# Performance work log

Hardware: AMD Instinct MI355X
Metric: run time of the kernel (lower is better)

Reference implementation:

```python
import jax, jax.numpy as jnp
import numpy as np

SG_SLOPE = 20.0  # fast_sigmoid surrogate slope
THRESHOLD = 1.0

@jax.custom_vjp
def spike_fn(v):
    # Heaviside spike with fast-sigmoid surrogate gradient
    return (v > 0).astype(v.dtype)

def _spike_fwd(v):
    return spike_fn(v), v

def _spike_bwd(v, g):
    return (g / (SG_SLOPE * jnp.abs(v) + 1.0) ** 2,)

spike_fn.defvjp(_spike_fwd, _spike_bwd)

def setup_inputs() -> dict:
    key = jax.random.key(0)
    T, IN, H, HEADS, O = 8192, 192, 1024, 5, 2
    dt = 0.004
    sp = float(np.log1p(np.exp(0.5413)))  # softplus(param) ~= 1.0
    tau_syn_h, tau_mem_h = 0.01 * sp, 0.02 * sp
    tau_syn_r = np.array([0.01, 0.02, 0.05, 0.1, 0.2]) * sp
    tau_mem_r = np.array([0.02, 0.05, 0.1, 0.2, 0.5]) * sp
    k1, k2, k3, k4 = jax.random.split(key, 4)
    x = jax.random.normal(k1, (T, IN), jnp.float32)
    W_in = jax.random.normal(k2, (H, IN), jnp.float32) / np.sqrt(IN)
    V = jax.random.normal(k3, (H, H), jnp.float32) / np.sqrt(H)
    b_rec = jnp.zeros((H,), jnp.float32)
    W_out = jax.random.normal(k4, (HEADS, O, H), jnp.float32) / np.sqrt(H)
    return {
        "x": x, "W_in": W_in, "V": V, "b_rec": b_rec, "W_out": W_out,
        "alpha_h": jnp.float32(np.exp(-dt / tau_syn_h)),
        "beta_h": jnp.float32(np.exp(-dt / tau_mem_h)),
        "alpha_r": jnp.asarray(np.exp(-dt / tau_syn_r), jnp.float32),
        "beta_r": jnp.asarray(np.exp(-dt / tau_mem_r), jnp.float32),
    }

def reference(x, W_in, V, b_rec, W_out, alpha_h, beta_h, alpha_r, beta_r):
    H = W_in.shape[0]
    HEADS, O, _ = W_out.shape
    dt_f32 = x.dtype

    def step(carry, x_t):
        inp_prev, spk, syn_h, mem_h, syn_r, mem_r = carry
        # hidden RSynaptic (note: fc_hidden consumes the PREVIOUS input, one-step delay)
        cur = W_in @ inp_prev + V @ spk + b_rec
        syn_h_new = alpha_h * syn_h + cur
        reset = jax.lax.stop_gradient(spk)  # zero-reset uses previous spike, detached
        mem_h_new = (beta_h * mem_h + syn_h_new) * (1.0 - reset)
        spk_new = spike_fn(mem_h_new - THRESHOLD)
        # readout heads consume the PREVIOUS hidden spike (pre-update)
        r_in = jnp.einsum("hoc,c->ho", W_out, spk)  # [HEADS, 2]
        syn_r_new = alpha_r[:, None] * syn_r + r_in
        mem_r_new = beta_r[:, None] * mem_r + syn_r_new  # reset_mechanism='none'
        out = mem_r_new.mean(axis=0)  # average over readout heads
        return (x_t, spk_new, syn_h_new, mem_h_new, syn_r_new, mem_r_new), out

    init = (
        jnp.zeros_like(x[0]),
        jnp.zeros((H,), dt_f32),
        jnp.zeros((H,), dt_f32),
        jnp.zeros((H,), dt_f32),
        jnp.zeros((HEADS, O), dt_f32),
        jnp.zeros((HEADS, O), dt_f32),
    )
    _, preds = jax.lax.scan(step, init, x)
    return preds  # [T, 2]
```

## Files before the change

### kernel.cpp

```cpp
#include <hip/hip_runtime.h>
#include <hip/hip_bf16.h>


constexpr int T_STEPS = 8192;
constexpr int IN_DIM  = 192;
constexpr int H_DIM   = 1024;
constexpr int NBLK    = 32;
constexpr int RING    = 4;

__global__ void k_clear(unsigned int* __restrict__ p, int n) {
    int i = blockIdx.x * blockDim.x + threadIdx.x;
    if (i < n) p[i] = 0u;
}

__global__ __launch_bounds__(576, 1) void k_phase1(
    const float* __restrict__ x,
    const float* __restrict__ W_in,
    const float* __restrict__ V,
    const float* __restrict__ b_rec,
    const float* __restrict__ alpha_h_p,
    const float* __restrict__ beta_h_p,
    unsigned long long* __restrict__ mbox,
    uint2* __restrict__ raster)
{
    const int tid   = threadIdx.x;
    const int blk   = blockIdx.x;
    const int w     = tid >> 6;
    const int l     = tid & 63;
    const bool syncw = (w == 8);
    const int r_local = l >> 4;
    const int cg      = l & 15;
    const int row   = (blk << 5) + (w << 2) + r_local;

    __shared__ unsigned int       bits_lds[2][NBLK];
    __shared__ unsigned long long combine[2];

    if (tid < NBLK) { bits_lds[0][tid] = 0u; bits_lds[1][tid] = 0u; }
    if (tid == 0)   { combine[0] = 0ull; combine[1] = 0ull; }

    float4 vfrag[16];
    float  wfrag[12];
    float  b_r = 0.f;
    if (!syncw) {
        const float4* vp = (const float4*)(V + (size_t)row * H_DIM + cg * 64);
        #pragma unroll
        for (int i = 0; i < 16; ++i) vfrag[i] = vp[i];
        const float* wp = W_in + row * IN_DIM + cg * 12;
        #pragma unroll
        for (int i = 0; i < 12; ++i) wfrag[i] = wp[i];
        b_r = b_rec[row];
    }
    const float ah = alpha_h_p[0];
    const float bh = beta_h_p[0];

    const float* xptr = x + cg * 12;
    float xr[12];
    #pragma unroll
    for (int i = 0; i < 12; ++i) xr[i] = 0.0f;

    float syn = 0.f, mem = 0.f, prev = 0.f;

    __syncthreads();

    for (int t = 0; t < T_STEPS; ++t) {
        const int rs  = (t + 1) & 1;
        const int wsl = t & 1;

        if (!syncw) {
            const float4* xp4 = (const float4*)xptr;
            float4 f0 = xp4[0], f1 = xp4[1], f2 = xp4[2];

            unsigned int b0 = bits_lds[rs][2 * cg];
            unsigned int b1 = bits_lds[rs][2 * cg + 1];

            float a0 = 0.f, a1 = 0.f;
            #pragma unroll
            for (int i = 0; i < 8; ++i) {
                a0 = fmaf((float)((b0 >> (4 * i + 0)) & 1u), vfrag[i].x, a0);
                a0 = fmaf((float)((b0 >> (4 * i + 1)) & 1u), vfrag[i].y, a0);
                a0 = fmaf((float)((b0 >> (4 * i + 2)) & 1u), vfrag[i].z, a0);
                a0 = fmaf((float)((b0 >> (4 * i + 3)) & 1u), vfrag[i].w, a0);
                a1 = fmaf((float)((b1 >> (4 * i + 0)) & 1u), vfrag[8 + i].x, a1);
                a1 = fmaf((float)((b1 >> (4 * i + 1)) & 1u), vfrag[8 + i].y, a1);
                a1 = fmaf((float)((b1 >> (4 * i + 2)) & 1u), vfrag[8 + i].z, a1);
                a1 = fmaf((float)((b1 >> (4 * i + 3)) & 1u), vfrag[8 + i].w, a1);
            }
            #pragma unroll
            for (int i = 0; i < 12; ++i) a0 = fmaf(wfrag[i], xr[i], a0);
            float acc = a0 + a1;

            #pragma unroll
            for (int m = 1; m < 16; m <<= 1) acc += __shfl_xor(acc, m, 64);

            float cur = acc + b_r;
            syn = fmaf(ah, syn, cur);
            mem = fmaf(bh, mem, syn) * (1.0f - prev);
            float spk = (mem > 1.0f) ? 1.0f : 0.0f;
            prev = spk;

            unsigned long long bal = __ballot(spk > 0.5f);
            unsigned int isLast = 0u, bitsAll = 0u;
            if (l == 0) {
                unsigned int nib = (unsigned int)(bal & 1ull)
                                 | ((unsigned int)((bal >> 16) & 1ull) << 1)
                                 | ((unsigned int)((bal >> 32) & 1ull) << 2)
                                 | ((unsigned int)((bal >> 48) & 1ull) << 3);
                unsigned long long add =
                    (1ull << 32) | ((unsigned long long)nib << (4 * w));
                unsigned long long old = __hip_atomic_fetch_add(&combine[wsl], add,
                        __ATOMIC_RELAXED, __HIP_MEMORY_SCOPE_WORKGROUP);
                unsigned long long nv = old + add;
                if ((nv >> 32) == 8ull) { isLast = 1u; bitsAll = (unsigned int)nv; }
            }
            isLast = __shfl(isLast, 0, 64);
            if (isLast) {
                unsigned int bits = __shfl(bitsAll, 0, 64);
                unsigned int want = (unsigned int)(t + 1);
                unsigned int w0 = (want << 16) | (bits & 0xffffu);
                unsigned int w1 = (want << 16) | (bits >> 16);
                unsigned long long pack =
                    (unsigned long long)w0 | ((unsigned long long)w1 << 32);
                if (l < NBLK && l != blk) {
                    __hip_atomic_store(
                        &mbox[(size_t)(((t & (RING - 1)) * NBLK + l) * NBLK + blk)],
                        pack, __ATOMIC_RELAXED, __HIP_MEMORY_SCOPE_AGENT);
                }
                if (l == 0) {
                    raster[(size_t)t * NBLK + blk] = make_uint2(w0, w1);
                    bits_lds[wsl][blk] = bits;
                    combine[wsl] = 0ull;
                }
            }

            #pragma unroll
            for (int i = 0; i < 4; ++i) {
                xr[i]     = (&f0.x)[i];
                xr[4 + i] = (&f1.x)[i];
                xr[8 + i] = (&f2.x)[i];
            }
            xptr += IN_DIM;
        } else {
            if (t + 1 < T_STEPS) {
                const bool act = (l < NBLK) && (l != blk);
                const unsigned int want = (unsigned int)(t + 1);
                const unsigned long long* p =
                    &mbox[(size_t)(((t & (RING - 1)) * NBLK + blk) * NBLK + l)];
                unsigned long long vv = 0ull;
                bool ok = !act;
                if (act) {
                    vv = __hip_atomic_load(p, __ATOMIC_RELAXED,
                                           __HIP_MEMORY_SCOPE_AGENT);
                    ok = (((vv >> 16) & 0xffffull) == want) && ((vv >> 48) == want);
                }
                while (__any(!ok)) {
                    if (!ok) {
                        vv = __hip_atomic_load(p, __ATOMIC_RELAXED,
                                               __HIP_MEMORY_SCOPE_AGENT);
                        ok = (((vv >> 16) & 0xffffull) == want) && ((vv >> 48) == want);
                    }
                }
                if (act)
                    bits_lds[wsl][l] = (unsigned int)(vv & 0xffffull)
                                     | ((unsigned int)((vv >> 32) & 0xffffull) << 16);
            }
        }

        asm volatile("s_waitcnt lgkmcnt(0)" ::: "memory");
        __builtin_amdgcn_s_barrier();
        __builtin_amdgcn_sched_barrier(0);
    }
}

__global__ __launch_bounds__(256, 1) void k_readout_mm(
    const uint2* __restrict__ raster,
    const float* __restrict__ W_out,
    float* __restrict__ R)
{
    __shared__ float wlds[10 * 1033];
    for (int i = threadIdx.x; i < 10 * 1024; i += 256) {
        int r = i >> 10, c = i & 1023;
        wlds[r * 1033 + c] = W_out[i];
    }
    __syncthreads();

    int tid = threadIdx.x;
    if (tid >= 250) return;
    int tl = tid / 10, rowr = tid - tl * 10;
    int t = blockIdx.x * 25 + tl;
    if (t >= T_STEPS) return;

    float acc = 0.f;
    if (t > 0) {
        const uint2* wp = raster + (size_t)(t - 1) * NBLK;
        const float* wr = &wlds[rowr * 1033];
        for (int ww = 0; ww < NBLK; ++ww) {
            uint2 v = wp[ww];
            unsigned int bits = (v.x & 0xffffu) | ((v.y & 0xffffu) << 16);
            const float* wb = wr + ww * 32;
            #pragma unroll
            for (int j = 0; j < 32; ++j)
                acc = fmaf((float)((bits >> j) & 1u), wb[j], acc);
        }
    }
    R[t * 10 + rowr] = acc;
}

__global__ void k_scan(const float* __restrict__ R,
                       const float* __restrict__ alpha_r,
                       const float* __restrict__ beta_r,
                       float* __restrict__ memr_all)
{
    int lane = threadIdx.x;
    bool act = lane < 10;
    float a = act ? alpha_r[lane >> 1] : 0.f;
    float b = act ? beta_r[lane >> 1] : 0.f;
    float syn = 0.f, mem = 0.f;
    constexpr int PF = 8;
    float buf[PF];
    #pragma unroll
    for (int i = 0; i < PF; ++i) buf[i] = act ? R[i * 10 + lane] : 0.f;

    for (int tb = 0; tb < T_STEPS; tb += PF) {
        #pragma unroll
        for (int i = 0; i < PF; ++i) {
            int t = tb + i;
            syn = fmaf(a, syn, buf[i]);
            mem = fmaf(b, mem, syn);
            if (act) memr_all[t * 10 + lane] = mem;
            int tn = t + PF;
            buf[i] = (act && tn < T_STEPS) ? R[tn * 10 + lane] : 0.f;
        }
    }
}

__global__ void k_mean(const float* __restrict__ memr_all, float* __restrict__ out) {
    int g = blockIdx.x * blockDim.x + threadIdx.x;
    if (g >= T_STEPS * 2) return;
    int t = g >> 1, o = g & 1;
    const float* m = memr_all + t * 10 + o;
    out[g] = 0.2f * (m[0] + m[2] + m[4] + m[6] + m[8]);
}

extern "C" void kernel_launch(void* const* d_in, const int* in_sizes, int n_in,
                              void* d_out, int out_size, void* d_ws, size_t ws_size,
                              hipStream_t stream) {
    (void)in_sizes; (void)n_in; (void)out_size; (void)ws_size;
    const float* x       = (const float*)d_in[0];
    const float* W_in    = (const float*)d_in[1];
    const float* V       = (const float*)d_in[2];
    const float* b_rec   = (const float*)d_in[3];
    const float* W_out   = (const float*)d_in[4];
    const float* alpha_h = (const float*)d_in[5];
    const float* beta_h  = (const float*)d_in[6];
    const float* alpha_r = (const float*)d_in[7];
    const float* beta_r  = (const float*)d_in[8];
    float* out = (float*)d_out;

    char* wsb = (char*)d_ws;
    unsigned long long* mbox = (unsigned long long*)wsb;
    uint2* raster  = (uint2*)(wsb + RING * NBLK * NBLK * 8);
    float* Rbuf    = (float*)(wsb + RING * NBLK * NBLK * 8
                              + (size_t)T_STEPS * NBLK * 8);
    float* memr_all = Rbuf + (size_t)T_STEPS * 10;

    int nclr = RING * NBLK * NBLK * 2;
    k_clear<<<(nclr + 255) / 256, 256, 0, stream>>>((unsigned int*)mbox, nclr);
    k_phase1<<<NBLK, 576, 0, stream>>>(x, W_in, V, b_rec, alpha_h, beta_h,
                                       mbox, raster);
    k_readout_mm<<<(T_STEPS + 24) / 25, 256, 0, stream>>>(raster, W_out, Rbuf);
    k_scan<<<1, 64, 0, stream>>>(Rbuf, alpha_r, beta_r, memr_all);
    k_mean<<<(T_STEPS * 2 + 255) / 256, 256, 0, stream>>>(memr_all, out);
}
```

Baseline: 19.12 ms.

## Replace per-step workgroup barrier with LDS ready-flag handshake and deeper ring

Removes the per-timestep s_barrier between the sync wave and the compute waves. Readiness is now signalled through a packed LDS flag: the sync wave publishes how many steps of remote bits have arrived, and the last compute wave publishes its local bits. Spike bits are held in a 4-slot LDS ring so the sync wave can run ahead of the compute waves. Spin loops contain dummy FMAs, apparently to keep the waves busy while waiting, and the relaxed ordering adds some risk of correctness issues under memory reordering.

Result: faster. 17.78 ms (-7.0%).

```diff
diff --git a/kernel.cpp b/kernel.cpp
--- a/kernel.cpp
+++ b/kernel.cpp
@@ -32,11 +32,15 @@
     const int cg      = l & 15;
     const int row   = (blk << 5) + (w << 2) + r_local;
 
-    __shared__ unsigned int       bits_lds[2][NBLK];
+    __shared__ unsigned int       bits_lds[RING][NBLK];
     __shared__ unsigned long long combine[2];
-
-    if (tid < NBLK) { bits_lds[0][tid] = 0u; bits_lds[1][tid] = 0u; }
-    if (tid == 0)   { combine[0] = 0ull; combine[1] = 0ull; }
+    __shared__ unsigned long long rdyPack;
+
+    for (int i = tid; i < RING * NBLK; i += 576)
+        ((unsigned int*)bits_lds)[i] = 0u;
+    if (tid == 0) { combine[0] = 0ull; combine[1] = 0ull; rdyPack = 0ull; }
+
+    unsigned int* rp = (unsigned int*)&rdyPack;
 
     float4 vfrag[16];
     float  wfrag[12];
@@ -53,25 +57,69 @@
     const float ah = alpha_h_p[0];
     const float bh = beta_h_p[0];
 
-    const float* xptr = x + cg * 12;
-    float xr[12];
-    #pragma unroll
-    for (int i = 0; i < 12; ++i) xr[i] = 0.0f;
-
-    float syn = 0.f, mem = 0.f, prev = 0.f;
-
     __syncthreads();
 
-    for (int t = 0; t < T_STEPS; ++t) {
-        const int rs  = (t + 1) & 1;
-        const int wsl = t & 1;
-
-        if (!syncw) {
+    float u0 = 1.02f, u1 = 1.03f, u2 = 1.05f, u3 = 1.07f;
+    const float bc = 1.0000001f, bd = 1e-30f;
+
+    if (syncw) {
+        const bool act = (l < NBLK) && (l != blk);
+        for (int t = 0; t < T_STEPS - 1; ++t) {
+            const unsigned int want = (unsigned int)(t + 1);
+            const unsigned long long good =
+                ((unsigned long long)want << 16) | ((unsigned long long)want << 48);
+            const unsigned long long* p =
+                &mbox[(size_t)(((t & (RING - 1)) * NBLK + blk) * NBLK + l)];
+            unsigned long long vv = act
+                ? __hip_atomic_load(p, __ATOMIC_RELAXED, __HIP_MEMORY_SCOPE_AGENT)
+                : good;
+            bool ok = (((vv >> 16) & 0xffffull) == want) && ((vv >> 48) == want);
+            while (__any(!ok)) {
+                if (!ok)
+                    vv = __hip_atomic_load(p, __ATOMIC_RELAXED,
+                                           __HIP_MEMORY_SCOPE_AGENT);
+                #pragma unroll
+                for (int i = 0; i < 8; ++i) {
+                    u0 = fmaf(u0, bc, bd); u1 = fmaf(u1, bc, bd);
+                    u2 = fmaf(u2, bc, bd); u3 = fmaf(u3, bc, bd);
+                }
+                ok = (((vv >> 16) & 0xffffull) == want) && ((vv >> 48) == want);
+            }
+            if (act)
+                bits_lds[t & (RING - 1)][l] =
+                    (unsigned int)(vv & 0xffffull)
+                    | ((unsigned int)((vv >> 32) & 0xffffull) << 16);
+            if (l == 0)
+                __hip_atomic_store(&rp[0], (unsigned int)(t + 1),
+                                   __ATOMIC_RELEASE, __HIP_MEMORY_SCOPE_WORKGROUP);
+        }
+    } else {
+        const float* xptr = x + cg * 12;
+        float xr[12];
+        #pragma unroll
+        for (int i = 0; i < 12; ++i) xr[i] = 0.0f;
+        float syn = 0.f, mem = 0.f, prev = 0.f;
+
+        for (int t = 0; t < T_STEPS; ++t) {
             const float4* xp4 = (const float4*)xptr;
             float4 f0 = xp4[0], f1 = xp4[1], f2 = xp4[2];
 
-            unsigned int b0 = bits_lds[rs][2 * cg];
-            unsigned int b1 = bits_lds[rs][2 * cg + 1];
+            unsigned long long rv = __hip_atomic_load(&rdyPack, __ATOMIC_ACQUIRE,
+                                        __HIP_MEMORY_SCOPE_WORKGROUP);
+            while ((unsigned int)rv < (unsigned int)t ||
+                   (unsigned int)(rv >> 32) < (unsigned int)t) {
+                #pragma unroll
+                for (int i = 0; i < 4; ++i) {
+                    u0 = fmaf(u0, bc, bd); u1 = fmaf(u1, bc, bd);
+                    u2 = fmaf(u2, bc, bd); u3 = fmaf(u3, bc, bd);
+                }
+                rv = __hip_atomic_load(&rdyPack, __ATOMIC_ACQUIRE,
+                                       __HIP_MEMORY_SCOPE_WORKGROUP);
+            }
+
+            const int slot = (t + RING - 1) & (RING - 1);
+            unsigned int b0 = bits_lds[slot][2 * cg];
+            unsigned int b1 = bits_lds[slot][2 * cg + 1];
 
             float a0 = 0.f, a1 = 0.f;
             #pragma unroll
@@ -107,8 +155,8 @@
                                  | ((unsigned int)((bal >> 48) & 1ull) << 3);
                 unsigned long long add =
                     (1ull << 32) | ((unsigned long long)nib << (4 * w));
-                unsigned long long old = __hip_atomic_fetch_add(&combine[wsl], add,
-                        __ATOMIC_RELAXED, __HIP_MEMORY_SCOPE_WORKGROUP);
+                unsigned long long old = __hip_atomic_fetch_add(&combine[t & 1],
+                        add, __ATOMIC_RELAXED, __HIP_MEMORY_SCOPE_WORKGROUP);
                 unsigned long long nv = old + add;
                 if ((nv >> 32) == 8ull) { isLast = 1u; bitsAll = (unsigned int)nv; }
             }
@@ -116,19 +164,22 @@
             if (isLast) {
                 unsigned int bits = __shfl(bitsAll, 0, 64);
                 unsigned int want = (unsigned int)(t + 1);
-                unsigned int w0 = (want << 16) | (bits & 0xffffu);
-                unsigned int w1 = (want << 16) | (bits >> 16);
+                unsigned int w0t = (want << 16) | (bits & 0xffffu);
+                unsigned int w1t = (want << 16) | (bits >> 16);
                 unsigned long long pack =
-                    (unsigned long long)w0 | ((unsigned long long)w1 << 32);
+                    (unsigned long long)w0t | ((unsigned long long)w1t << 32);
                 if (l < NBLK && l != blk) {
                     __hip_atomic_store(
                         &mbox[(size_t)(((t & (RING - 1)) * NBLK + l) * NBLK + blk)],
                         pack, __ATOMIC_RELAXED, __HIP_MEMORY_SCOPE_AGENT);
                 }
                 if (l == 0) {
-                    raster[(size_t)t * NBLK + blk] = make_uint2(w0, w1);
-                    bits_lds[wsl][blk] = bits;
-                    combine[wsl] = 0ull;
+                    raster[(size_t)t * NBLK + blk] = make_uint2(w0t, w1t);
+                    bits_lds[t & (RING - 1)][blk] = bits;
+                    combine[t & 1] = 0ull;
+                    __hip_atomic_store(&rp[1], (unsigned int)(t + 1),
+                                       __ATOMIC_RELEASE,
+                                       __HIP_MEMORY_SCOPE_WORKGROUP);
                 }
             }
 
@@ -139,36 +190,9 @@
                 xr[8 + i] = (&f2.x)[i];
             }
             xptr += IN_DIM;
-        } else {
-            if (t + 1 < T_STEPS) {
-                const bool act = (l < NBLK) && (l != blk);
-                const unsigned int want = (unsigned int)(t + 1);
-                const unsigned long long* p =
-                    &mbox[(size_t)(((t & (RING - 1)) * NBLK + blk) * NBLK + l)];
-                unsigned long long vv = 0ull;
-                bool ok = !act;
-                if (act) {
-                    vv = __hip_atomic_load(p, __ATOMIC_RELAXED,
-                                           __HIP_MEMORY_SCOPE_AGENT);
-                    ok = (((vv >> 16) & 0xffffull) == want) && ((vv >> 48) == want);
-                }
-                while (__any(!ok)) {
-                    if (!ok) {
-                        vv = __hip_atomic_load(p, __ATOMIC_RELAXED,
-                                               __HIP_MEMORY_SCOPE_AGENT);
-                        ok = (((vv >> 16) & 0xffffull) == want) && ((vv >> 48) == want);
-                    }
-                }
-                if (act)
-                    bits_lds[wsl][l] = (unsigned int)(vv & 0xffffull)
-                                     | ((unsigned int)((vv >> 32) & 0xffffull) << 16);
-            }
-        }
-
-        asm volatile("s_waitcnt lgkmcnt(0)" ::: "memory");
-        __builtin_amdgcn_s_barrier();
-        __builtin_amdgcn_sched_barrier(0);
-    }
+        }
+    }
+    asm volatile("" :: "v"(u0), "v"(u1), "v"(u2), "v"(u3));
 }
 
 __global__ __launch_bounds__(256, 1) void k_readout_mm(
```

## Co-locate recurrent workers on one XCD and poll mailboxes directly from compute waves

Applied to the files above, without the earlier changes.

Launches 256 blocks and picks the first XCD to gather 32 blocks; only those 32 run the recurrence, so all inter-block mailbox traffic stays within one XCD's L2. The dedicated sync wave and per-step workgroup barrier are removed. Every compute wave now polls the mailbox itself with sc0 loads and distributes the spike words by shuffle, and each block also writes its own slot. Spin loops add dummy FMAs, and the selection protocol relies on hardware XCC IDs and on 32 blocks fitting on one XCD.

New measurement: 26.76 ms. +40.0%, slower.

```diff
diff --git a/kernel.cpp b/kernel.cpp
--- a/kernel.cpp
+++ b/kernel.cpp
@@ -5,15 +5,16 @@
 constexpr int T_STEPS = 8192;
 constexpr int IN_DIM  = 192;
 constexpr int H_DIM   = 1024;
-constexpr int NBLK    = 32;
+constexpr int NWORK   = 32;
 constexpr int RING    = 4;
+constexpr int NSEL    = 256;
 
 __global__ void k_clear(unsigned int* __restrict__ p, int n) {
     int i = blockIdx.x * blockDim.x + threadIdx.x;
     if (i < n) p[i] = 0u;
 }
 
-__global__ __launch_bounds__(576, 1) void k_phase1(
+__global__ __launch_bounds__(512, 1) void k_phase1(
     const float* __restrict__ x,
     const float* __restrict__ W_in,
     const float* __restrict__ V,
@@ -21,37 +22,59 @@
     const float* __restrict__ alpha_h_p,
     const float* __restrict__ beta_h_p,
     unsigned long long* __restrict__ mbox,
+    unsigned int* __restrict__ sel,
     uint2* __restrict__ raster)
 {
-    const int tid   = threadIdx.x;
-    const int blk   = blockIdx.x;
-    const int w     = tid >> 6;
-    const int l     = tid & 63;
-    const bool syncw = (w == 8);
+    const int tid = threadIdx.x;
+    __shared__ unsigned int sh_rank, sh_win;
+    __shared__ unsigned long long combine[2];
+
+    unsigned int xcd;
+    asm("s_getreg_b32 %0, hwreg(HW_REG_XCC_ID)" : "=s"(xcd));
+    xcd &= 7u;
+
+    if (tid == 0) {
+        combine[0] = 0ull; combine[1] = 0ull;
+        unsigned int r = __hip_atomic_fetch_add(&sel[xcd], 1u,
+                             __ATOMIC_RELAXED, __HIP_MEMORY_SCOPE_AGENT);
+        sh_rank = r;
+        if (r == NWORK - 1) {
+            unsigned int exp0 = 0u;
+            __hip_atomic_compare_exchange_strong(&sel[8], &exp0, xcd + 1u,
+                __ATOMIC_RELEASE, __ATOMIC_RELAXED, __HIP_MEMORY_SCOPE_AGENT);
+        }
+        unsigned int wv;
+        do {
+            wv = __hip_atomic_load(&sel[8], __ATOMIC_ACQUIRE,
+                                   __HIP_MEMORY_SCOPE_AGENT);
+        } while (wv == 0u);
+        sh_win = wv;
+    }
+    __syncthreads();
+    if (sh_win != xcd + 1u || sh_rank >= (unsigned)NWORK) return;
+    const int me = (int)sh_rank;
+
+    const int w  = tid >> 6;
+    const int l  = tid & 63;
     const int r_local = l >> 4;
     const int cg      = l & 15;
-    const int row   = (blk << 5) + (w << 2) + r_local;
-
-    __shared__ unsigned int       bits_lds[2][NBLK];
-    __shared__ unsigned long long combine[2];
-
-    if (tid < NBLK) { bits_lds[0][tid] = 0u; bits_lds[1][tid] = 0u; }
-    if (tid == 0)   { combine[0] = 0ull; combine[1] = 0ull; }
+    const int row = (me << 5) + (w << 2) + r_local;
 
     float4 vfrag[16];
-    float  wfrag[12];
-    float  b_r = 0.f;
-    if (!syncw) {
+    {
         const float4* vp = (const float4*)(V + (size_t)row * H_DIM + cg * 64);
         #pragma unroll
         for (int i = 0; i < 16; ++i) vfrag[i] = vp[i];
+    }
+    float wfrag[12];
+    {
         const float* wp = W_in + row * IN_DIM + cg * 12;
         #pragma unroll
         for (int i = 0; i < 12; ++i) wfrag[i] = wp[i];
-        b_r = b_rec[row];
-    }
-    const float ah = alpha_h_p[0];
-    const float bh = beta_h_p[0];
+    }
+    const float b_r = b_rec[row];
+    const float ah  = alpha_h_p[0];
+    const float bh  = beta_h_p[0];
 
     const float* xptr = x + cg * 12;
     float xr[12];
@@ -60,115 +83,121 @@
 
     float syn = 0.f, mem = 0.f, prev = 0.f;
 
+    float u0 = 1.02f, u1 = 1.03f;
+    const float bc = 1.0000001f, bd = 1e-30f;
+
     __syncthreads();
 
     for (int t = 0; t < T_STEPS; ++t) {
-        const int rs  = (t + 1) & 1;
+        const float4* xp4 = (const float4*)xptr;
+        float4 f0 = xp4[0], f1 = xp4[1], f2 = xp4[2];
+
+        unsigned long long word = 0ull;
+        if (t > 0) {
+            const unsigned int want = (unsigned int)t;
+            const unsigned long long* pa =
+                &mbox[((size_t)((t - 1) & (RING - 1)) * NWORK + me) * NWORK + (l & 31)];
+            unsigned long long vv;
+            asm volatile("global_load_dwordx2 %0, %1, off sc0\n\t"
+                         "s_waitcnt vmcnt(0)"
+                         : "=&v"(vv) : "v"(pa) : "memory");
+            bool ok = (((unsigned int)(vv >> 16) & 0xffffu) == want) &&
+                      ((unsigned int)(vv >> 48) == want);
+            int spins = 0;
+            while (__any(!ok)) {
+                if (!ok) {
+                    if (++spins <= 6) {
+                        asm volatile("global_load_dwordx2 %0, %1, off sc0\n\t"
+                                     "s_waitcnt vmcnt(0)"
+                                     : "=&v"(vv) : "v"(pa) : "memory");
+                    } else {
+                        vv = __hip_atomic_load(pa, __ATOMIC_RELAXED,
+                                               __HIP_MEMORY_SCOPE_AGENT);
+                    }
+                    ok = (((unsigned int)(vv >> 16) & 0xffffu) == want) &&
+                         ((unsigned int)(vv >> 48) == want);
+                }
+                u0 = fmaf(u0, bc, bd); u1 = fmaf(u1, bc, bd);
+            }
+            word = vv;
+        }
+        unsigned long long p0 = __shfl(word, 2 * cg, 64);
+        unsigned long long p1 = __shfl(word, 2 * cg + 1, 64);
+        unsigned int b0 = ((unsigned int)p0 & 0xffffu)
+                        | (((unsigned int)(p0 >> 32) & 0xffffu) << 16);
+        unsigned int b1 = ((unsigned int)p1 & 0xffffu)
+                        | (((unsigned int)(p1 >> 32) & 0xffffu) << 16);
+
+        float a0 = 0.f, a1 = 0.f;
+        #pragma unroll
+        for (int i = 0; i < 8; ++i) {
+            a0 = fmaf((float)((b0 >> (4 * i + 0)) & 1u), vfrag[i].x, a0);
+            a0 = fmaf((float)((b0 >> (4 * i + 1)) & 1u), vfrag[i].y, a0);
+            a0 = fmaf((float)((b0 >> (4 * i + 2)) & 1u), vfrag[i].z, a0);
+            a0 = fmaf((float)((b0 >> (4 * i + 3)) & 1u), vfrag[i].w, a0);
+            a1 = fmaf((float)((b1 >> (4 * i + 0)) & 1u), vfrag[8 + i].x, a1);
+            a1 = fmaf((float)((b1 >> (4 * i + 1)) & 1u), vfrag[8 + i].y, a1);
+            a1 = fmaf((float)((b1 >> (4 * i + 2)) & 1u), vfrag[8 + i].z, a1);
+            a1 = fmaf((float)((b1 >> (4 * i + 3)) & 1u), vfrag[8 + i].w, a1);
+        }
+        #pragma unroll
+        for (int i = 0; i < 12; ++i) a0 = fmaf(wfrag[i], xr[i], a0);
+        float acc = a0 + a1;
+
+        #pragma unroll
+        for (int m = 1; m < 16; m <<= 1) acc += __shfl_xor(acc, m, 64);
+
+        float cur = acc + b_r;
+        syn = fmaf(ah, syn, cur);
+        mem = fmaf(bh, mem, syn) * (1.0f - prev);
+        float spk = (mem > 1.0f) ? 1.0f : 0.0f;
+        prev = spk;
+
         const int wsl = t & 1;
-
-        if (!syncw) {
-            const float4* xp4 = (const float4*)xptr;
-            float4 f0 = xp4[0], f1 = xp4[1], f2 = xp4[2];
-
-            unsigned int b0 = bits_lds[rs][2 * cg];
-            unsigned int b1 = bits_lds[rs][2 * cg + 1];
-
-            float a0 = 0.f, a1 = 0.f;
-            #pragma unroll
-            for (int i = 0; i < 8; ++i) {
-                a0 = fmaf((float)((b0 >> (4 * i + 0)) & 1u), vfrag[i].x, a0);
-                a0 = fmaf((float)((b0 >> (4 * i + 1)) & 1u), vfrag[i].y, a0);
-                a0 = fmaf((float)((b0 >> (4 * i + 2)) & 1u), vfrag[i].z, a0);
-                a0 = fmaf((float)((b0 >> (4 * i + 3)) & 1u), vfrag[i].w, a0);
-                a1 = fmaf((float)((b1 >> (4 * i + 0)) & 1u), vfrag[8 + i].x, a1);
-                a1 = fmaf((float)((b1 >> (4 * i + 1)) & 1u), vfrag[8 + i].y, a1);
-                a1 = fmaf((float)((b1 >> (4 * i + 2)) & 1u), vfrag[8 + i].z, a1);
-                a1 = fmaf((float)((b1 >> (4 * i + 3)) & 1u), vfrag[8 + i].w, a1);
+        unsigned long long bal = __ballot(spk > 0.5f);
+        unsigned int isLast = 0u, bitsAll = 0u;
+        if (l == 0) {
+            unsigned int nib = (unsigned int)(bal & 1ull)
+                             | ((unsigned int)((bal >> 16) & 1ull) << 1)
+                             | ((unsigned int)((bal >> 32) & 1ull) << 2)
+                             | ((unsigned int)((bal >> 48) & 1ull) << 3);
+            unsigned long long add =
+                (1ull << 32) | ((unsigned long long)nib << (4 * w));
+            unsigned long long old = __hip_atomic_fetch_add(&combine[wsl], add,
+                    __ATOMIC_RELAXED, __HIP_MEMORY_SCOPE_WORKGROUP);
+            unsigned long long nv = old + add;
+            if ((nv >> 32) == 8ull) { isLast = 1u; bitsAll = (unsigned int)nv; }
+        }
+        isLast = __shfl(isLast, 0, 64);
+        if (isLast) {
+            unsigned int bits = __shfl(bitsAll, 0, 64);
+            unsigned int want = (unsigned int)(t + 1);
+            unsigned int w0t = (want << 16) | (bits & 0xffffu);
+            unsigned int w1t = (want << 16) | (bits >> 16);
+            unsigned long long pack =
+                (unsigned long long)w0t | ((unsigned long long)w1t << 32);
+            if (l == 0) combine[wsl] = 0ull;
+            asm volatile("s_waitcnt lgkmcnt(0)" ::: "memory");
+            if (l < NWORK) {
+                unsigned long long* ps =
+                    &mbox[((size_t)(t & (RING - 1)) * NWORK + l) * NWORK + me];
+                asm volatile("global_store_dwordx2 %0, %1, off sc0"
+                             :: "v"(ps), "v"(pack) : "memory");
+                __hip_atomic_store(ps, pack, __ATOMIC_RELAXED,
+                                   __HIP_MEMORY_SCOPE_AGENT);
             }
-            #pragma unroll
-            for (int i = 0; i < 12; ++i) a0 = fmaf(wfrag[i], xr[i], a0);
-            float acc = a0 + a1;
-
-            #pragma unroll
-            for (int m = 1; m < 16; m <<= 1) acc += __shfl_xor(acc, m, 64);
-
-            float cur = acc + b_r;
-            syn = fmaf(ah, syn, cur);
-            mem = fmaf(bh, mem, syn) * (1.0f - prev);
-            float spk = (mem > 1.0f) ? 1.0f : 0.0f;
-            prev = spk;
-
-            unsigned long long bal = __ballot(spk > 0.5f);
-            unsigned int isLast = 0u, bitsAll = 0u;
-            if (l == 0) {
-                unsigned int nib = (unsigned int)(bal & 1ull)
-                                 | ((unsigned int)((bal >> 16) & 1ull) << 1)
-                                 | ((unsigned int)((bal >> 32) & 1ull) << 2)
-                                 | ((unsigned int)((bal >> 48) & 1ull) << 3);
-                unsigned long long add =
-                    (1ull << 32) | ((unsigned long long)nib << (4 * w));
-                unsigned long long old = __hip_atomic_fetch_add(&combine[wsl], add,
-                        __ATOMIC_RELAXED, __HIP_MEMORY_SCOPE_WORKGROUP);
-                unsigned long long nv = old + add;
-                if ((nv >> 32) == 8ull) { isLast = 1u; bitsAll = (unsigned int)nv; }
-            }
-            isLast = __shfl(isLast, 0, 64);
-            if (isLast) {
-                unsigned int bits = __shfl(bitsAll, 0, 64);
-                unsigned int want = (unsigned int)(t + 1);
-                unsigned int w0 = (want << 16) | (bits & 0xffffu);
-                unsigned int w1 = (want << 16) | (bits >> 16);
-                unsigned long long pack =
-                    (unsigned long long)w0 | ((unsigned long long)w1 << 32);
-                if (l < NBLK && l != blk) {
-                    __hip_atomic_store(
-                        &mbox[(size_t)(((t & (RING - 1)) * NBLK + l) * NBLK + blk)],
-                        pack, __ATOMIC_RELAXED, __HIP_MEMORY_SCOPE_AGENT);
-                }
-                if (l == 0) {
-                    raster[(size_t)t * NBLK + blk] = make_uint2(w0, w1);
-                    bits_lds[wsl][blk] = bits;
-                    combine[wsl] = 0ull;
-                }
-            }
-
-            #pragma unroll
-            for (int i = 0; i < 4; ++i) {
-                xr[i]     = (&f0.x)[i];
-                xr[4 + i] = (&f1.x)[i];
-                xr[8 + i] = (&f2.x)[i];
-            }
-            xptr += IN_DIM;
-        } else {
-            if (t + 1 < T_STEPS) {
-                const bool act = (l < NBLK) && (l != blk);
-                const unsigned int want = (unsigned int)(t + 1);
-                const unsigned long long* p =
-                    &mbox[(size_t)(((t & (RING - 1)) * NBLK + blk) * NBLK + l)];
-                unsigned long long vv = 0ull;
-                bool ok = !act;
-                if (act) {
-                    vv = __hip_atomic_load(p, __ATOMIC_RELAXED,
-                                           __HIP_MEMORY_SCOPE_AGENT);
-                    ok = (((vv >> 16) & 0xffffull) == want) && ((vv >> 48) == want);
-                }
-                while (__any(!ok)) {
-                    if (!ok) {
-                        vv = __hip_atomic_load(p, __ATOMIC_RELAXED,
-                                               __HIP_MEMORY_SCOPE_AGENT);
-                        ok = (((vv >> 16) & 0xffffull) == want) && ((vv >> 48) == want);
-                    }
-                }
-                if (act)
-                    bits_lds[wsl][l] = (unsigned int)(vv & 0xffffull)
-                                     | ((unsigned int)((vv >> 32) & 0xffffull) << 16);
-            }
-        }
-
-        asm volatile("s_waitcnt lgkmcnt(0)" ::: "memory");
-        __builtin_amdgcn_s_barrier();
-        __builtin_amdgcn_sched_barrier(0);
-    }
+            if (l == 0) raster[(size_t)t * NWORK + me] = make_uint2(w0t, w1t);
+        }
+
+        #pragma unroll
+        for (int i = 0; i < 4; ++i) {
+            xr[i]     = (&f0.x)[i];
+            xr[4 + i] = (&f1.x)[i];
+            xr[8 + i] = (&f2.x)[i];
+        }
+        xptr += IN_DIM;
+    }
+    asm volatile("" :: "v"(u0), "v"(u1));
 }
 
 __global__ __launch_bounds__(256, 1) void k_readout_mm(
@@ -191,9 +220,9 @@
 
     float acc = 0.f;
     if (t > 0) {
-        const uint2* wp = raster + (size_t)(t - 1) * NBLK;
+        const uint2* wp = raster + (size_t)(t - 1) * NWORK;
         const float* wr = &wlds[rowr * 1033];
-        for (int ww = 0; ww < NBLK; ++ww) {
+        for (int ww = 0; ww < NWORK; ++ww) {
             uint2 v = wp[ww];
             unsigned int bits = (v.x & 0xffffu) | ((v.y & 0xffffu) << 16);
             const float* wb = wr + ww * 32;
@@ -258,15 +287,16 @@
 
     char* wsb = (char*)d_ws;
     unsigned long long* mbox = (unsigned long long*)wsb;
-    uint2* raster  = (uint2*)(wsb + RING * NBLK * NBLK * 8);
-    float* Rbuf    = (float*)(wsb + RING * NBLK * NBLK * 8
-                              + (size_t)T_STEPS * NBLK * 8);
+    unsigned int* selp = (unsigned int*)(wsb + RING * NWORK * NWORK * 8);
+    uint2* raster  = (uint2*)(wsb + RING * NWORK * NWORK * 8 + 64);
+    float* Rbuf    = (float*)(wsb + RING * NWORK * NWORK * 8 + 64
+                              + (size_t)T_STEPS * NWORK * 8);
     float* memr_all = Rbuf + (size_t)T_STEPS * 10;
 
-    int nclr = RING * NBLK * NBLK * 2;
+    int nclr = RING * NWORK * NWORK * 2 + 16;
     k_clear<<<(nclr + 255) / 256, 256, 0, stream>>>((unsigned int*)mbox, nclr);
-    k_phase1<<<NBLK, 576, 0, stream>>>(x, W_in, V, b_rec, alpha_h, beta_h,
-                                       mbox, raster);
+    k_phase1<<<NSEL, 512, 0, stream>>>(x, W_in, V, b_rec, alpha_h, beta_h,
+                                       mbox, selp, raster);
     k_readout_mm<<<(T_STEPS + 24) / 25, 256, 0, stream>>>(raster, W_out, Rbuf);
     k_scan<<<1, 64, 0, stream>>>(Rbuf, alpha_r, beta_r, memr_all);
     k_mean<<<(T_STEPS * 2 + 255) / 256, 256, 0, stream>>>(memr_all, out);
```
